# Kernel tuning notes

Hardware: AMD Instinct MI355X
Metric: run time of the kernel (lower is better)

## Reference

```python
import jax, jax.numpy as jnp
import numpy as np


def log_g(x):
    # log of g(x) = where(x>=0, x+0.5, sigmoid(x))
    return jnp.where(x >= 0, jnp.log(jax.nn.relu(x) + 0.5), -jax.nn.softplus(-x))


def setup_inputs() -> dict:
    key = jax.random.key(0)
    ks = jax.random.split(key, 6)
    B, S, D, Din = 4, 4096, 1024, 2048
    x = jax.random.normal(ks[0], (B, S, D), jnp.float32)
    s1 = 1.0 / np.sqrt(D)
    W1 = jax.random.normal(ks[1], (D, 3 * Din), jnp.float32) * s1
    b1 = jax.random.normal(ks[2], (3 * Din,), jnp.float32) * s1
    b1 = b1.at[Din:2 * Din].add(1.0)  # forget_bias_init_scale = 1.0
    s2 = 1.0 / np.sqrt(Din)
    W2 = jax.random.normal(ks[3], (Din, D), jnp.float32) * s2
    b2 = jax.random.normal(ks[4], (D,), jnp.float32) * s2
    init_h = jax.random.normal(ks[5], (Din,), jnp.float32)
    return {"x": x, "W1": W1, "b1": b1, "W2": W2, "b2": b2, "init_h": init_h}


def reference(x, W1, b1, W2, b2, init_h):
    B, S, _ = x.shape
    Din = init_h.shape[0]
    proj = x @ W1 + b1                              # [B,S,3*Din]
    hidden, forget_gate, input_gate = jnp.split(proj, 3, axis=-1)
    # use_coeff_norm = True branch (normalized gates in log space)
    diff = jax.nn.softplus(-forget_gate) - jax.nn.softplus(-input_gate)
    log_coeffs = -jax.nn.softplus(diff)             # log(f/(f+i))
    log_val_coeffs = -jax.nn.softplus(-diff)        # log(i/(f+i))
    log_values = log_val_coeffs + log_g(hidden)     # [B,S,Din]
    # prepend learned initial hidden state
    prev_log_hidden = jnp.broadcast_to(log_g(init_h), (B, 1, Din))
    log_values = jnp.concatenate([prev_log_hidden, log_values], axis=1)  # [B,S+1,Din]
    log_coeffs = jnp.pad(log_coeffs, ((0, 0), (1, 0), (0, 0)))           # [B,S+1,Din]
    # heinsen associative scan in log space
    a_star = jnp.cumsum(log_coeffs, axis=1)
    log_h = a_star + jax.lax.cumlogsumexp(log_values - a_star, axis=1)
    out_h = jnp.exp(log_h[:, -S:])                  # [B,S,Din]
    next_hidden = out_h[:, -1:]
    next_log_hidden = log_h[:, -1:]
    out = out_h @ W2 + b2                           # [B,S,D]
    return (out, next_hidden, next_log_hidden)
```

## Files before the change

### kernel.cpp

```cpp
#include <hip/hip_runtime.h>
#include <cstdint>
#include <cstddef>

#define BB 4
#define SS 4096
#define DD 1024
#define DIN 2048
#define MTOT (BB*SS)
#define K1 DD
#define K2 DIN
#define N2 DD
#define NCH (BB*DIN)
#define NCHUNK 32
#define CLEN (SS/NCHUNK)

typedef _Float16 half8  __attribute__((ext_vector_type(8)));
typedef _Float16 half4v __attribute__((ext_vector_type(4)));
typedef float    floatx4 __attribute__((ext_vector_type(4)));

#define AS1(p) ((__attribute__((address_space(1))) void*)(uintptr_t)(p))
#define AS3(p) ((__attribute__((address_space(3))) void*)(uint32_t)(uintptr_t)(p))

__device__ __forceinline__ void gload16(const void* g, void* l) {
  __builtin_amdgcn_global_load_lds(AS1(g), AS3(l), 16, 0, 0);
}

__device__ __forceinline__ float sigm(float x) { return 1.f / (1.f + __expf(-x)); }
__device__ __forceinline__ uint32_t hbits(float f) {
  _Float16 h = (_Float16)f; uint16_t u; __builtin_memcpy(&u, &h, 2); return (uint32_t)u;
}
__device__ __forceinline__ float h_lo(uint32_t v) {
  uint16_t u = (uint16_t)(v & 0xffffu); _Float16 h; __builtin_memcpy(&h, &u, 2); return (float)h;
}
__device__ __forceinline__ float h_hi(uint32_t v) {
  uint16_t u = (uint16_t)(v >> 16); _Float16 h; __builtin_memcpy(&h, &u, 2); return (float)h;
}


__global__ void f32_to_f16_vec(const float* __restrict__ src, _Float16* __restrict__ dst) {
  int i = (blockIdx.x * blockDim.x + threadIdx.x) * 4;
  float4 v = *(const float4*)(src + i);
  half4v o; o.x = (_Float16)v.x; o.y = (_Float16)v.y; o.z = (_Float16)v.z; o.w = (_Float16)v.w;
  *(half4v*)(dst + i) = o;
}

__global__ void transpose_cvt(const float* __restrict__ src, _Float16* __restrict__ dst,
                              int R, int C) {
  __shared__ float t[32][33];
  int c0 = blockIdx.x * 32, r0 = blockIdx.y * 32;
  int tx = threadIdx.x, ty = threadIdx.y;
#pragma unroll
  for (int j = 0; j < 32; j += 8)
    t[ty + j][tx] = src[(size_t)(r0 + ty + j) * C + c0 + tx];
  __syncthreads();
#pragma unroll
  for (int j = 0; j < 32; j += 8)
    dst[(size_t)(c0 + ty + j) * R + r0 + tx] = (_Float16)t[tx][ty + j];
}

__global__ __launch_bounds__(256) void gemm1_fused(
    const _Float16* __restrict__ xh, const _Float16* __restrict__ w1t,
    const float* __restrict__ b1, uint32_t* __restrict__ zg) {
  __shared__ _Float16 As[3][128 * 32];
  __shared__ _Float16 Bs[2][3][64 * 32];

  const int tid = threadIdx.x;
  const int wave = tid >> 6, lane = tid & 63;
  const int wm = wave >> 1, wn = wave & 1;
  const int m0 = blockIdx.y * 128;
  const int d0 = blockIdx.x * 64;
  const int lrow = lane >> 2;
  const int lk = (((lane & 3) ^ ((lrow >> 1) & 3)) * 8);
  const int roff = ((((lane & 15) << 2) | ((lane >> 4) ^ ((lane >> 1) & 3))) * 8);

  const _Float16* pA0 = xh + (size_t)(m0 + (wave * 2 + 0) * 16 + lrow) * K1 + lk;
  const _Float16* pA1 = pA0 + (size_t)16 * K1;
  const _Float16* pB0 = w1t + (size_t)(d0 + wave * 16 + lrow) * K1 + lk;
  const _Float16* pB1 = pB0 + (size_t)DIN * K1;
  const _Float16* pB2 = pB1 + (size_t)DIN * K1;

  floatx4 acc[3][4][2] = {};

  gload16(pB0, &Bs[0][0][wave * 512]);
  gload16(pB1, &Bs[0][1][wave * 512]);
  gload16(pB2, &Bs[0][2][wave * 512]);
  gload16(pA0, &As[0][(wave * 2 + 0) * 512]);
  gload16(pA1, &As[0][(wave * 2 + 1) * 512]);
  gload16(pA0 + 32, &As[1][(wave * 2 + 0) * 512]);
  gload16(pA1 + 32, &As[1][(wave * 2 + 1) * 512]);
  pB0 += 32; pB1 += 32; pB2 += 32;
  pA0 += 64; pA1 += 64;

#define G1_STEP(rbA, sbA, rbB, sbB)                                             \
  do {                                                                          \
    asm volatile("s_waitcnt vmcnt(2)" ::: "memory");                            \
    __builtin_amdgcn_s_barrier();                                               \
    asm volatile("" ::: "memory");                                              \
    gload16(pB0, &Bs[sbB][0][wave * 512]);                                      \
    gload16(pB1, &Bs[sbB][1][wave * 512]);                                      \
    gload16(pB2, &Bs[sbB][2][wave * 512]);                                      \
    gload16(pA0, &As[sbA][(wave * 2 + 0) * 512]);                               \
    gload16(pA1, &As[sbA][(wave * 2 + 1) * 512]);                               \
    pA0 += 32; pA1 += 32; pB0 += 32; pB1 += 32; pB2 += 32;                      \
    half8 af[4], bfr[3][2];                                                     \
    _Pragma("unroll")                                                           \
    for (int mi = 0; mi < 4; ++mi)                                              \
      af[mi] = *(const half8*)(&As[rbA][(wm * 4 + mi) * 512 + roff]);           \
    _Pragma("unroll")                                                           \
    for (int gt = 0; gt < 3; ++gt)                                              \
      _Pragma("unroll")                                                         \
      for (int ni = 0; ni < 2; ++ni)                                            \
        bfr[gt][ni] = *(const half8*)(&Bs[rbB][gt][(wn * 2 + ni) * 512 + roff]);\
    _Pragma("unroll")                                                           \
    for (int gt = 0; gt < 3; ++gt)                                              \
      _Pragma("unroll")                                                         \
      for (int mi = 0; mi < 4; ++mi)                                            \
        _Pragma("unroll")                                                       \
        for (int ni = 0; ni < 2; ++ni)                                          \
          acc[gt][mi][ni] = __builtin_amdgcn_mfma_f32_16x16x32_f16(             \
              af[mi], bfr[gt][ni], acc[gt][mi][ni], 0, 0, 0);                   \
  } while (0)

  for (int it6 = 0; it6 < 5; ++it6) {
    G1_STEP(0, 2, 0, 1);
    G1_STEP(1, 0, 1, 0);
    G1_STEP(2, 1, 0, 1);
    G1_STEP(0, 2, 1, 0);
    G1_STEP(1, 0, 0, 1);
    G1_STEP(2, 1, 1, 0);
  }
  G1_STEP(0, 2, 0, 1);
  G1_STEP(1, 0, 1, 0);
#undef G1_STEP

#pragma unroll
  for (int ni = 0; ni < 2; ++ni) {
    int d = d0 + wn * 32 + ni * 16 + (lane & 15);
    float bh = b1[d], bf_ = b1[DIN + d], bi = b1[2 * DIN + d];
#pragma unroll
    for (int mi = 0; mi < 4; ++mi) {
#pragma unroll
      for (int r = 0; r < 4; ++r) {
        int m = m0 + wm * 64 + mi * 16 + (lane >> 4) * 4 + r;
        float hv = acc[0][mi][ni][r] + bh;
        float fv = acc[1][mi][ni][r] + bf_;
        float iv = acc[2][mi][ni][r] + bi;
        float u = 1.f + __expf(-fminf(fmaxf(fv, -30.f), 30.f));
        float v = 1.f + __expf(-fminf(fmaxf(iv, -30.f), 30.f));
        float z = __fdividef(u, u + v);
        float gg = (hv >= 0.f) ? (hv + 0.5f)
                               : __fdividef(1.f, 1.f + __expf(-fmaxf(hv, -30.f)));
        zg[(size_t)m * DIN + d] = hbits(z) | (hbits(gg) << 16);
      }
    }
  }
}


__global__ void scanA(const uint32_t* __restrict__ zg,
                      float* __restrict__ cA, float* __restrict__ cB) {
  int gidx = blockIdx.x * 256 + threadIdx.x;
  int q = gidx >> 13, c = gidx & (NCH - 1);
  int b = c >> 11, d = c & (DIN - 1);
  size_t base = ((size_t)b * SS + q * CLEN) * DIN + d;
  float A = 1.f, Bv = 0.f;
#pragma unroll 4
  for (int t = 0; t < CLEN; ++t) {
    uint32_t v = zg[base + (size_t)t * DIN];
    float z = h_lo(v), g = h_hi(v);
    A *= (1.f - z);
    Bv = fmaf(z, g - Bv, Bv);
  }
  cA[q * NCH + c] = A;
  cB[q * NCH + c] = Bv;
}

__global__ void scanB(const float* __restrict__ cA, const float* __restrict__ cB,
                      const float* __restrict__ init_h, float* __restrict__ cH) {
  int c = blockIdx.x * 256 + threadIdx.x;
  int d = c & (DIN - 1);
  float x = init_h[d];
  float h = (x >= 0.f) ? (x + 0.5f) : sigm(x);
#pragma unroll
  for (int q = 0; q < NCHUNK; ++q) {
    cH[q * NCH + c] = h;
    h = fmaf(cA[q * NCH + c], h, cB[q * NCH + c]);
  }
}

__global__ void scanC(const uint32_t* __restrict__ zg, const float* __restrict__ cH,
                      _Float16* __restrict__ hh, float* __restrict__ out_tail) {
  int gidx = blockIdx.x * 256 + threadIdx.x;
  int q = gidx >> 13, c = gidx & (NCH - 1);
  int b = c >> 11, d = c & (DIN - 1);
  size_t base = ((size_t)b * SS + q * CLEN) * DIN + d;
  float h = cH[q * NCH + c];
#pragma unroll 4
  for (int t = 0; t < CLEN; ++t) {
    uint32_t v = zg[base + (size_t)t * DIN];
    float z = h_lo(v), g = h_hi(v);
    h = fmaf(z, g - h, h);
    hh[base + (size_t)t * DIN] = (_Float16)h;
  }
  if (q == NCHUNK - 1) {
    out_tail[c] = h;
    out_tail[NCH + c] = logf(h);
  }
}

__global__ __launch_bounds__(256, 4) void gemm2k(
    const _Float16* __restrict__ hh, const _Float16* __restrict__ w2t,
    const float* __restrict__ b2, float* __restrict__ out) {
  __shared__ _Float16 As[2][128 * 32];
  __shared__ _Float16 Bs[2][128 * 32];

  const int tid = threadIdx.x;
  const int wave = tid >> 6, lane = tid & 63;
  const int wm = wave >> 1, wn = wave & 1;
  const int m0 = blockIdx.y * 128;
  const int n0 = blockIdx.x * 128;
  const int lrow = lane >> 2;
  const int lk = (((lane & 3) ^ ((lrow >> 1) & 3)) * 8);
  const int roff = ((((lane & 15) << 2) | ((lane >> 4) ^ ((lane >> 1) & 3))) * 8);

  const _Float16* pA0 = hh + (size_t)(m0 + (wave * 2 + 0) * 16 + lrow) * K2 + lk;
  const _Float16* pA1 = pA0 + (size_t)16 * K2;
  const _Float16* pB0 = w2t + (size_t)(n0 + (wave * 2 + 0) * 16 + lrow) * K2 + lk;
  const _Float16* pB1 = pB0 + (size_t)16 * K2;

  floatx4 acc[4][4] = {};

  gload16(pA0, &As[0][(wave * 2 + 0) * 512]);
  gload16(pA1, &As[0][(wave * 2 + 1) * 512]);
  gload16(pB0, &Bs[0][(wave * 2 + 0) * 512]);
  gload16(pB1, &Bs[0][(wave * 2 + 1) * 512]);
  pA0 += 32; pA1 += 32; pB0 += 32; pB1 += 32;

#define G2_STEP(rb, sb)                                                         \
  do {                                                                          \
    asm volatile("s_waitcnt vmcnt(0)" ::: "memory");                            \
    __builtin_amdgcn_s_barrier();                                               \
    asm volatile("" ::: "memory");                                              \
    gload16(pA0, &As[sb][(wave * 2 + 0) * 512]);                                \
    gload16(pA1, &As[sb][(wave * 2 + 1) * 512]);                                \
    gload16(pB0, &Bs[sb][(wave * 2 + 0) * 512]);                                \
    gload16(pB1, &Bs[sb][(wave * 2 + 1) * 512]);                                \
    pA0 += 32; pA1 += 32; pB0 += 32; pB1 += 32;                                 \
    half8 af[4], bfr[4];                                                        \
    _Pragma("unroll")                                                           \
    for (int mi = 0; mi < 4; ++mi)                                              \
      af[mi] = *(const half8*)(&As[rb][(wm * 4 + mi) * 512 + roff]);            \
    _Pragma("unroll")                                                           \
    for (int ni = 0; ni < 4; ++ni)                                              \
      bfr[ni] = *(const half8*)(&Bs[rb][(wn * 4 + ni) * 512 + roff]);           \
    _Pragma("unroll")                                                           \
    for (int mi = 0; mi < 4; ++mi)                                              \
      _Pragma("unroll")                                                         \
      for (int ni = 0; ni < 4; ++ni)                                            \
        acc[mi][ni] = __builtin_amdgcn_mfma_f32_16x16x32_f16(                   \
            af[mi], bfr[ni], acc[mi][ni], 0, 0, 0);                             \
  } while (0)

  for (int it2 = 0; it2 < 32; ++it2) {
    G2_STEP(0, 1);
    G2_STEP(1, 0);
  }
#undef G2_STEP

#pragma unroll
  for (int ni = 0; ni < 4; ++ni) {
    int n = n0 + wn * 64 + ni * 16 + (lane & 15);
    float bias = b2[n];
#pragma unroll
    for (int mi = 0; mi < 4; ++mi) {
#pragma unroll
      for (int r = 0; r < 4; ++r) {
        int m = m0 + wm * 64 + mi * 16 + (lane >> 4) * 4 + r;
        out[(size_t)m * N2 + n] = acc[mi][ni][r] + bias;
      }
    }
  }
}


extern "C" void kernel_launch(void* const* d_in, const int* in_sizes, int n_in,
                              void* d_out, int out_size, void* d_ws, size_t ws_size,
                              hipStream_t stream) {
  const float* x      = (const float*)d_in[0];
  const float* W1     = (const float*)d_in[1];
  const float* b1     = (const float*)d_in[2];
  const float* W2     = (const float*)d_in[3];
  const float* b2     = (const float*)d_in[4];
  const float* init_h = (const float*)d_in[5];
  float* out = (float*)d_out;

  char* w = (char*)d_ws;
  _Float16* xh  = (_Float16*)w; w += (size_t)MTOT * K1 * 2;
  _Float16* w1t = (_Float16*)w; w += (size_t)3 * DIN * K1 * 2;
  _Float16* w2t = (_Float16*)w; w += (size_t)N2 * K2 * 2;
  uint32_t* zg  = (uint32_t*)w; w += (size_t)MTOT * DIN * 4;
  _Float16* hh  = (_Float16*)w; w += (size_t)MTOT * DIN * 2;
  float* cA = (float*)w; w += (size_t)NCH * NCHUNK * 4;
  float* cB = (float*)w; w += (size_t)NCH * NCHUNK * 4;
  float* cH = (float*)w; w += (size_t)NCH * NCHUNK * 4;

  f32_to_f16_vec<<<dim3(MTOT * K1 / 1024), dim3(256), 0, stream>>>(x, xh);
  transpose_cvt<<<dim3(3 * DIN / 32, K1 / 32), dim3(32, 8), 0, stream>>>(W1, w1t, K1, 3 * DIN);
  transpose_cvt<<<dim3(N2 / 32, K2 / 32), dim3(32, 8), 0, stream>>>(W2, w2t, K2, N2);

  gemm1_fused<<<dim3(DIN / 64, MTOT / 128), dim3(256), 0, stream>>>(xh, w1t, b1, zg);

  scanA<<<dim3(NCH * NCHUNK / 256), dim3(256), 0, stream>>>(zg, cA, cB);
  scanB<<<dim3(NCH / 256), dim3(256), 0, stream>>>(cA, cB, init_h, cH);
  scanC<<<dim3(NCH * NCHUNK / 256), dim3(256), 0, stream>>>(zg, cH, hh, out + (size_t)MTOT * DD);

  gemm2k<<<dim3(N2 / 128, MTOT / 128), dim3(256), 0, stream>>>(hh, w2t, b2, out);
}
```

Baseline: 542.1 us.

## Double M tile to 256 rows with 512-thread blocks in both GEMMs

Both GEMMs move from 256-thread blocks with 128-row M tiles to 512-thread blocks with 256-row M tiles. The weight (B) tile is now shared by twice as many rows, which cuts redundant global loads of W1 and W2. In gemm1 only the first four waves stage B. gemm2 also switches to a triple-buffered A ring with a vmcnt(2) wait instead of vmcnt(0), so loads overlap compute more deeply. The tighter launch bounds (512,4 for gemm2 and 512,2 for gemm1) limit per-thread registers, which risks accumulator spills, and the larger LDS footprint lowers the number of blocks per CU.

```diff
diff --git a/kernel.cpp b/kernel.cpp
--- a/kernel.cpp
+++ b/kernel.cpp
@@ -58,32 +58,35 @@
     dst[(size_t)(c0 + ty + j) * R + r0 + tx] = (_Float16)t[tx][ty + j];
 }
 
-__global__ __launch_bounds__(256) void gemm1_fused(
+__global__ __launch_bounds__(512, 2) void gemm1_fused(
     const _Float16* __restrict__ xh, const _Float16* __restrict__ w1t,
     const float* __restrict__ b1, uint32_t* __restrict__ zg) {
-  __shared__ _Float16 As[3][128 * 32];
+  __shared__ _Float16 As[3][256 * 32];
   __shared__ _Float16 Bs[2][3][64 * 32];
 
   const int tid = threadIdx.x;
   const int wave = tid >> 6, lane = tid & 63;
   const int wm = wave >> 1, wn = wave & 1;
-  const int m0 = blockIdx.y * 128;
+  const int m0 = blockIdx.y * 256;
   const int d0 = blockIdx.x * 64;
   const int lrow = lane >> 2;
   const int lk = (((lane & 3) ^ ((lrow >> 1) & 3)) * 8);
   const int roff = ((((lane & 15) << 2) | ((lane >> 4) ^ ((lane >> 1) & 3))) * 8);
-
-  const _Float16* pA0 = xh + (size_t)(m0 + (wave * 2 + 0) * 16 + lrow) * K1 + lk;
+  const bool bstage = (wave < 4);
+
+  const _Float16* pA0 = xh + (size_t)(m0 + wave * 32 + lrow) * K1 + lk;
   const _Float16* pA1 = pA0 + (size_t)16 * K1;
-  const _Float16* pB0 = w1t + (size_t)(d0 + wave * 16 + lrow) * K1 + lk;
+  const _Float16* pB0 = w1t + (size_t)(d0 + (wave & 3) * 16 + lrow) * K1 + lk;
   const _Float16* pB1 = pB0 + (size_t)DIN * K1;
   const _Float16* pB2 = pB1 + (size_t)DIN * K1;
 
   floatx4 acc[3][4][2] = {};
 
-  gload16(pB0, &Bs[0][0][wave * 512]);
-  gload16(pB1, &Bs[0][1][wave * 512]);
-  gload16(pB2, &Bs[0][2][wave * 512]);
+  if (bstage) {
+    gload16(pB0, &Bs[0][0][wave * 512]);
+    gload16(pB1, &Bs[0][1][wave * 512]);
+    gload16(pB2, &Bs[0][2][wave * 512]);
+  }
   gload16(pA0, &As[0][(wave * 2 + 0) * 512]);
   gload16(pA1, &As[0][(wave * 2 + 1) * 512]);
   gload16(pA0 + 32, &As[1][(wave * 2 + 0) * 512]);
@@ -96,9 +99,11 @@
     asm volatile("s_waitcnt vmcnt(2)" ::: "memory");                            \
     __builtin_amdgcn_s_barrier();                                               \
     asm volatile("" ::: "memory");                                              \
-    gload16(pB0, &Bs[sbB][0][wave * 512]);                                      \
-    gload16(pB1, &Bs[sbB][1][wave * 512]);                                      \
-    gload16(pB2, &Bs[sbB][2][wave * 512]);                                      \
+    if (bstage) {                                                               \
+      gload16(pB0, &Bs[sbB][0][wave * 512]);                                    \
+      gload16(pB1, &Bs[sbB][1][wave * 512]);                                    \
+      gload16(pB2, &Bs[sbB][2][wave * 512]);                                    \
+    }                                                                           \
     gload16(pA0, &As[sbA][(wave * 2 + 0) * 512]);                               \
     gload16(pA1, &As[sbA][(wave * 2 + 1) * 512]);                               \
     pA0 += 32; pA1 += 32; pB0 += 32; pB1 += 32; pB2 += 32;                      \
@@ -208,51 +213,51 @@
   }
 }
 
-__global__ __launch_bounds__(256, 4) void gemm2k(
+__global__ __launch_bounds__(512, 4) void gemm2k(
     const _Float16* __restrict__ hh, const _Float16* __restrict__ w2t,
     const float* __restrict__ b2, float* __restrict__ out) {
-  __shared__ _Float16 As[2][128 * 32];
+  __shared__ _Float16 As[3][256 * 32];
   __shared__ _Float16 Bs[2][128 * 32];
 
   const int tid = threadIdx.x;
   const int wave = tid >> 6, lane = tid & 63;
   const int wm = wave >> 1, wn = wave & 1;
-  const int m0 = blockIdx.y * 128;
+  const int m0 = blockIdx.y * 256;
   const int n0 = blockIdx.x * 128;
   const int lrow = lane >> 2;
   const int lk = (((lane & 3) ^ ((lrow >> 1) & 3)) * 8);
   const int roff = ((((lane & 15) << 2) | ((lane >> 4) ^ ((lane >> 1) & 3))) * 8);
 
-  const _Float16* pA0 = hh + (size_t)(m0 + (wave * 2 + 0) * 16 + lrow) * K2 + lk;
+  const _Float16* pA0 = hh + (size_t)(m0 + wave * 32 + lrow) * K2 + lk;
   const _Float16* pA1 = pA0 + (size_t)16 * K2;
-  const _Float16* pB0 = w2t + (size_t)(n0 + (wave * 2 + 0) * 16 + lrow) * K2 + lk;
-  const _Float16* pB1 = pB0 + (size_t)16 * K2;
+  const _Float16* pB0 = w2t + (size_t)(n0 + wave * 16 + lrow) * K2 + lk;
 
   floatx4 acc[4][4] = {};
 
+  gload16(pB0, &Bs[0][wave * 512]);
   gload16(pA0, &As[0][(wave * 2 + 0) * 512]);
   gload16(pA1, &As[0][(wave * 2 + 1) * 512]);
-  gload16(pB0, &Bs[0][(wave * 2 + 0) * 512]);
-  gload16(pB1, &Bs[0][(wave * 2 + 1) * 512]);
-  pA0 += 32; pA1 += 32; pB0 += 32; pB1 += 32;
-
-#define G2_STEP(rb, sb)                                                         \
+  gload16(pA0 + 32, &As[1][(wave * 2 + 0) * 512]);
+  gload16(pA1 + 32, &As[1][(wave * 2 + 1) * 512]);
+  pB0 += 32;
+  pA0 += 64; pA1 += 64;
+
+#define G2_STEP(rbA, sbA, rbB, sbB)                                             \
   do {                                                                          \
-    asm volatile("s_waitcnt vmcnt(0)" ::: "memory");                            \
+    asm volatile("s_waitcnt vmcnt(2)" ::: "memory");                            \
     __builtin_amdgcn_s_barrier();                                               \
     asm volatile("" ::: "memory");                                              \
-    gload16(pA0, &As[sb][(wave * 2 + 0) * 512]);                                \
-    gload16(pA1, &As[sb][(wave * 2 + 1) * 512]);                                \
-    gload16(pB0, &Bs[sb][(wave * 2 + 0) * 512]);                                \
-    gload16(pB1, &Bs[sb][(wave * 2 + 1) * 512]);                                \
-    pA0 += 32; pA1 += 32; pB0 += 32; pB1 += 32;                                 \
+    gload16(pB0, &Bs[sbB][wave * 512]);                                         \
+    gload16(pA0, &As[sbA][(wave * 2 + 0) * 512]);                               \
+    gload16(pA1, &As[sbA][(wave * 2 + 1) * 512]);                               \
+    pA0 += 32; pA1 += 32; pB0 += 32;                                            \
     half8 af[4], bfr[4];                                                        \
     _Pragma("unroll")                                                           \
     for (int mi = 0; mi < 4; ++mi)                                              \
-      af[mi] = *(const half8*)(&As[rb][(wm * 4 + mi) * 512 + roff]);            \
+      af[mi] = *(const half8*)(&As[rbA][(wm * 4 + mi) * 512 + roff]);           \
     _Pragma("unroll")                                                           \
     for (int ni = 0; ni < 4; ++ni)                                              \
-      bfr[ni] = *(const half8*)(&Bs[rb][(wn * 4 + ni) * 512 + roff]);           \
+      bfr[ni] = *(const half8*)(&Bs[rbB][(wn * 4 + ni) * 512 + roff]);          \
     _Pragma("unroll")                                                           \
     for (int mi = 0; mi < 4; ++mi)                                              \
       _Pragma("unroll")                                                         \
@@ -261,10 +266,18 @@
             af[mi], bfr[ni], acc[mi][ni], 0, 0, 0);                             \
   } while (0)
 
-  for (int it2 = 0; it2 < 32; ++it2) {
-    G2_STEP(0, 1);
-    G2_STEP(1, 0);
-  }
+  for (int it6 = 0; it6 < 10; ++it6) {
+    G2_STEP(0, 2, 0, 1);
+    G2_STEP(1, 0, 1, 0);
+    G2_STEP(2, 1, 0, 1);
+    G2_STEP(0, 2, 1, 0);
+    G2_STEP(1, 0, 0, 1);
+    G2_STEP(2, 1, 1, 0);
+  }
+  G2_STEP(0, 2, 0, 1);
+  G2_STEP(1, 0, 1, 0);
+  G2_STEP(2, 1, 0, 1);
+  G2_STEP(0, 2, 1, 0);
 #undef G2_STEP
 
 #pragma unroll
@@ -308,11 +321,11 @@
   transpose_cvt<<<dim3(3 * DIN / 32, K1 / 32), dim3(32, 8), 0, stream>>>(W1, w1t, K1, 3 * DIN);
   transpose_cvt<<<dim3(N2 / 32, K2 / 32), dim3(32, 8), 0, stream>>>(W2, w2t, K2, N2);
 
-  gemm1_fused<<<dim3(DIN / 64, MTOT / 128), dim3(256), 0, stream>>>(xh, w1t, b1, zg);
+  gemm1_fused<<<dim3(DIN / 64, MTOT / 256), dim3(512), 0, stream>>>(xh, w1t, b1, zg);
 
   scanA<<<dim3(NCH * NCHUNK / 256), dim3(256), 0, stream>>>(zg, cA, cB);
   scanB<<<dim3(NCH / 256), dim3(256), 0, stream>>>(cA, cB, init_h, cH);
   scanC<<<dim3(NCH * NCHUNK / 256), dim3(256), 0, stream>>>(zg, cH, hh, out + (size_t)MTOT * DD);
 
-  gemm2k<<<dim3(N2 / 128, MTOT / 128), dim3(256), 0, stream>>>(hh, w2t, b2, out);
-}
+  gemm2k<<<dim3(N2 / 128, MTOT / 256), dim3(512), 0, stream>>>(hh, w2t, b2, out);
+}
```

After: 541.1 us. Within noise of the previous version (-0.2%).
